# Optimization experiments

Measured on AMD Instinct MI355X. Metric: run time of the kernel, lower is better.

Reference implementation:

```python
import jax, jax.numpy as jnp
import numpy as np

EPS = 1e-06
H, D_MODEL = 16, 1024
DK = D_MODEL // H
B, S = 16, 4096


def elu_fea_map(x):
    return jax.nn.elu(x) + 1.0


def setup_inputs() -> dict:
    key = jax.random.key(0)
    ks = jax.random.split(key, 11)
    lim = 1.0 / np.sqrt(D_MODEL)
    u = lambda k, shp: jax.random.uniform(k, shp, jnp.float32, -lim, lim)
    return {
        "query": jax.random.normal(ks[0], (B, D_MODEL), jnp.float32),
        "key": jax.random.normal(ks[1], (B, S, D_MODEL), jnp.float32),
        "value": jax.random.normal(ks[2], (B, S, D_MODEL), jnp.float32),
        "Wq": u(ks[3], (D_MODEL, D_MODEL)), "bq": u(ks[4], (D_MODEL,)),
        "Wk": u(ks[5], (D_MODEL, D_MODEL)), "bk": u(ks[6], (D_MODEL,)),
        "Wv": u(ks[7], (D_MODEL, D_MODEL)), "bv": u(ks[8], (D_MODEL,)),
        "Wo": u(ks[9], (D_MODEL, D_MODEL)), "bo": u(ks[10], (D_MODEL,)),
    }


def reference(query, key, value, Wq, bq, Wk, bk, Wv, bv, Wo, bo):
    nb = query.shape[0]
    # projections; torch Linear: x @ W.T + b
    q = (query @ Wq.T + bq).reshape(nb, 1, H, DK)   # [B,1,H,D]
    k = (key @ Wk.T + bk).reshape(nb, -1, H, DK)    # [B,S,H,D]
    v = (value @ Wv.T + bv).reshape(nb, -1, H, DK)  # [B,S,H,M]
    Q = elu_fea_map(q)
    K = elu_fea_map(k)
    KV = jnp.einsum('bshd,bshm->bhdm', K, v)                      # [B,H,D,M]
    Z = 1.0 / (jnp.einsum('bshd,bhd->bsh', Q, K.sum(axis=1)) + EPS)  # [B,1,H]
    V = jnp.einsum('bshd,bhdm,bsh->bshm', Q, KV, Z)               # [B,1,H,M]
    x = V.reshape(nb, H * DK)
    return x @ Wo.T + bo
```

## Files before the change

kernel.cpp:

```cpp
#include <hip/hip_runtime.h>
#include <hip/hip_bf16.h>
#include <stdint.h>


using bf16 = __hip_bfloat16;
typedef __attribute__((ext_vector_type(8))) short short8;
typedef __attribute__((ext_vector_type(4))) float f32x4;

#define NB_B 16
#define SEQ 4096
#define DM 1024
#define NH 16
#define DKH 64

__device__ __forceinline__ void gload_lds16(const void* g, void* l) {
  __builtin_amdgcn_global_load_lds((const __attribute__((address_space(1))) void*)g,
                                   (__attribute__((address_space(3))) void*)l, 16, 0, 0);
}

__global__ __launch_bounds__(256) void conv_kernel(const float* __restrict__ src,
                                                   bf16* __restrict__ dst, long n4) {
  long i = (long)blockIdx.x * blockDim.x + threadIdx.x;
  const long stride = (long)gridDim.x * blockDim.x;
  for (; i < n4; i += stride) {
    float4 v = ((const float4*)src)[i];
    union { ushort4 u; bf16 h[4]; } o;
    o.h[0] = __float2bfloat16(v.x);
    o.h[1] = __float2bfloat16(v.y);
    o.h[2] = __float2bfloat16(v.z);
    o.h[3] = __float2bfloat16(v.w);
    ((ushort4*)dst)[i] = o.u;
  }
}

template <int KPROJ>
__global__ __launch_bounds__(256) void gemm_proj(
    const float* __restrict__ A, const bf16* __restrict__ W,
    const float* __restrict__ bias, bf16* __restrict__ outT,
    float* __restrict__ Ksum, int rowsTot, int b0, int chunk) {
  __shared__ bf16 As[128 * 64];
  __shared__ bf16 Bs[128 * 64];
  const int tid = threadIdx.x;
  const int lane = tid & 63;
  const int wid = tid >> 6;
  const int wr = wid >> 1, wc = wid & 1;
  const int wgid = (blockIdx.x & 7) * chunk + (blockIdx.x >> 3);
  const int row0 = (wgid >> 3) * 128;
  const int col0 = (wgid & 7) * 128;
  f32x4 acc[4][4] = {};

  char* AsB = (char*)As;
  const int str = tid >> 3;
  const int sslotA = ((tid & 7) ^ (str & 7));
  const int bsrc = (((lane & 7) ^ (lane >> 3)) * 8);
  const int xr = (lane & 7) << 4;
  const int lr = lane & 15;
  const int lk = (lane >> 4) * 16;

  for (int kt = 0; kt < DM / 64; ++kt) {
    const int kb = kt * 64;
#pragma unroll
    for (int i = 0; i < 4; ++i)
      gload_lds16(W + (long)(col0 + wid * 32 + i * 8 + (lane >> 3)) * DM + kb + bsrc,
                  &Bs[(wid * 4 + i) * 512]);
    float4 fa[4][2];
#pragma unroll
    for (int i = 0; i < 4; ++i) {
      const float* src = A + (long)(row0 + i * 32 + str) * DM + kb + (tid & 7) * 8;
      fa[i][0] = *(const float4*)src;
      fa[i][1] = *(const float4*)(src + 4);
    }
#pragma unroll
    for (int i = 0; i < 4; ++i) {
      union { bf16 h[8]; short8 v; } pk;
      pk.h[0] = __float2bfloat16(fa[i][0].x);
      pk.h[1] = __float2bfloat16(fa[i][0].y);
      pk.h[2] = __float2bfloat16(fa[i][0].z);
      pk.h[3] = __float2bfloat16(fa[i][0].w);
      pk.h[4] = __float2bfloat16(fa[i][1].x);
      pk.h[5] = __float2bfloat16(fa[i][1].y);
      pk.h[6] = __float2bfloat16(fa[i][1].z);
      pk.h[7] = __float2bfloat16(fa[i][1].w);
      *(short8*)(AsB + (i * 32 + str) * 128 + (sslotA << 4)) = pk.v;
    }
    __syncthreads();
#pragma unroll
    for (int kk = 0; kk < 2; ++kk) {
      short8 af[4], bfv[4];
#pragma unroll
      for (int m = 0; m < 4; ++m) {
        const int row = wr * 64 + m * 16 + lr;
        af[m] = *(const short8*)(AsB + row * 128 + ((kk * 64 + lk) ^ xr));
      }
#pragma unroll
      for (int n = 0; n < 4; ++n) {
        const int row = wc * 64 + n * 16 + lr;
        bfv[n] = *(const short8*)((char*)Bs + row * 128 + ((kk * 64 + lk) ^ xr));
      }
#pragma unroll
      for (int m = 0; m < 4; ++m)
#pragma unroll
        for (int n = 0; n < 4; ++n)
          acc[m][n] = __builtin_amdgcn_mfma_f32_16x16x32_bf16(af[m], bfv[n], acc[m][n], 0, 0, 0);
    }
    __syncthreads();
  }

  const int bglob = b0 + (row0 >> 12);
#pragma unroll
  for (int n = 0; n < 4; ++n) {
    const int colg = col0 + wc * 64 + n * 16 + (lane & 15);
    const float bv = bias[colg];
    float csum = 0.f;
#pragma unroll
    for (int m = 0; m < 4; ++m) {
      const int r = row0 + wr * 64 + m * 16 + (lane >> 4) * 4;
      union { ushort4 u; bf16 h[4]; } pk;
#pragma unroll
      for (int i = 0; i < 4; ++i) {
        float v = acc[m][n][i] + bv;
        if (KPROJ) { v = v > 0.f ? v + 1.f : __expf(v); csum += v; }
        pk.h[i] = __float2bfloat16(v);
      }
      *(ushort4*)&outT[(long)colg * rowsTot + r] = pk.u;
    }
    if (KPROJ) {
      csum += __shfl_xor(csum, 16);
      csum += __shfl_xor(csum, 32);
      if (lane < 16) atomicAdd(&Ksum[(long)bglob * DM + colg], csum);
    }
  }
}

__global__ __launch_bounds__(256) void kv_kernel(
    const bf16* __restrict__ KT, const bf16* __restrict__ VT,
    float* __restrict__ KVp, int rowsTot, int b0) {
  const int sp = blockIdx.x & 3;
  const int h = (blockIdx.x >> 2) & 15;
  const int b_loc = blockIdx.x >> 6;
  const int lane = threadIdx.x & 63;
  const int w = threadIdx.x >> 6;
  const long srow = (long)b_loc * SEQ + sp * (SEQ / 4) + ((lane >> 4) * 8);
  const bf16* Ab = KT + (long)(h * DKH + w * 16 + (lane & 15)) * rowsTot + srow;
  const bf16* Bb = VT + (long)(h * DKH + (lane & 15)) * rowsTot + srow;
  f32x4 acc[4] = {};
#pragma unroll 2
  for (int s = 0; s < SEQ / 4; s += 32) {
    short8 a = *(const short8*)(Ab + s);
#pragma unroll
    for (int n = 0; n < 4; ++n) {
      short8 bv = *(const short8*)(Bb + (long)n * 16 * rowsTot + s);
      acc[n] = __builtin_amdgcn_mfma_f32_16x16x32_bf16(a, bv, acc[n], 0, 0, 0);
    }
  }
  float* o = KVp + (((long)sp * NB_B + (b0 + b_loc)) * NH + h) * DKH * DKH;
#pragma unroll
  for (int n = 0; n < 4; ++n)
#pragma unroll
    for (int i = 0; i < 4; ++i)
      o[(w * 16 + (lane >> 4) * 4 + i) * DKH + n * 16 + (lane & 15)] = acc[n][i];
}

template <int ELU>
__global__ __launch_bounds__(256) void vecmat_kernel(
    const float* __restrict__ in, const float* __restrict__ W,
    const float* __restrict__ bias, float* __restrict__ outp) {
  const int b = blockIdx.x >> 5;
  const int n0 = (blockIdx.x & 31) * 32;
  const int lane = threadIdx.x & 63;
  const int w = threadIdx.x >> 6;
  float4 qv[4];
#pragma unroll
  for (int it = 0; it < 4; ++it)
    qv[it] = *(const float4*)&in[(long)b * DM + it * 256 + lane * 4];
#pragma unroll
  for (int j = 0; j < 8; ++j) {
    const int n = n0 + w * 8 + j;
    const float* wrow = W + (long)n * DM;
    float s = 0.f;
#pragma unroll
    for (int it = 0; it < 4; ++it) {
      float4 wv = *(const float4*)&wrow[it * 256 + lane * 4];
      s += qv[it].x * wv.x + qv[it].y * wv.y + qv[it].z * wv.z + qv[it].w * wv.w;
    }
    s += __shfl_xor(s, 1);  s += __shfl_xor(s, 2);  s += __shfl_xor(s, 4);
    s += __shfl_xor(s, 8);  s += __shfl_xor(s, 16); s += __shfl_xor(s, 32);
    if (lane == 0) {
      float v = s + bias[n];
      if (ELU) v = v > 0.f ? v + 1.f : __expf(v);
      outp[(long)b * DM + n] = v;
    }
  }
}

__global__ __launch_bounds__(256) void xcomp_kernel(
    const float* __restrict__ Q, const float* __restrict__ KVp,
    const float* __restrict__ Ksum, float* __restrict__ xb) {
  const int b = blockIdx.x;
  const int t = threadIdx.x;
  const int h = t >> 4;
  const int m0 = (t & 15) * 4;
  const float* q = Q + (long)b * DM + h * DKH;
  const float* ks = Ksum + (long)b * DM + h * DKH;
  const long kvoff = ((long)b * NH + h) * DKH * DKH;
  const long spstride = (long)NB_B * NH * DKH * DKH;
  float zden = 0.f;
#pragma unroll
  for (int d = 0; d < DKH; ++d) zden += q[d] * ks[d];
  const float z = 1.f / (zden + 1e-6f);
  float nv[4] = {0.f, 0.f, 0.f, 0.f};
  for (int d = 0; d < DKH; ++d) {
    const float qd = q[d];
#pragma unroll
    for (int j = 0; j < 4; ++j) {
      const long idx = kvoff + d * DKH + m0 + j;
      nv[j] += qd * (KVp[idx] + KVp[idx + spstride] +
                     KVp[idx + 2 * spstride] + KVp[idx + 3 * spstride]);
    }
  }
  float* xo = xb + (long)b * DM + h * DKH + m0;
#pragma unroll
  for (int j = 0; j < 4; ++j) xo[j] = nv[j] * z;
}

extern "C" void kernel_launch(void* const* d_in, const int* in_sizes, int n_in,
                              void* d_out, int out_size, void* d_ws, size_t ws_size,
                              hipStream_t stream) {
  (void)in_sizes; (void)n_in; (void)out_size;
  const float* query = (const float*)d_in[0];
  const float* key   = (const float*)d_in[1];
  const float* value = (const float*)d_in[2];
  const float* Wq = (const float*)d_in[3];
  const float* bq = (const float*)d_in[4];
  const float* Wk = (const float*)d_in[5];
  const float* bk = (const float*)d_in[6];
  const float* Wv = (const float*)d_in[7];
  const float* bv = (const float*)d_in[8];
  const float* Wo = (const float*)d_in[9];
  const float* bo = (const float*)d_in[10];
  float* out = (float*)d_out;

  char* p = (char*)d_ws;
  bf16* WkB = (bf16*)p;  p += (size_t)DM * DM * 2;
  bf16* WvB = (bf16*)p;  p += (size_t)DM * DM * 2;
  float* KVp = (float*)p; p += (size_t)4 * NB_B * NH * DKH * DKH * 4;
  float* Ksum = (float*)p; p += (size_t)NB_B * DM * 4;
  float* Q = (float*)p;  p += (size_t)NB_B * DM * 4;
  float* xb = (float*)p; p += (size_t)NB_B * DM * 4;
  const size_t fixed = (size_t)(p - (char*)d_ws);
  const size_t per_b = (size_t)2 * SEQ * DM * 2;
  if (ws_size < fixed + per_b) return;
  int nbc = (int)((ws_size - fixed) / per_b);
  if (nbc > NB_B) nbc = NB_B;
  bf16* kT = (bf16*)p; p += (size_t)nbc * SEQ * DM * 2;
  bf16* vT = (bf16*)p; p += (size_t)nbc * SEQ * DM * 2;

  hipMemsetAsync(Ksum, 0, (size_t)NB_B * DM * 4, stream);
  conv_kernel<<<512, 256, 0, stream>>>(Wk, WkB, (long)DM * DM / 4);
  conv_kernel<<<512, 256, 0, stream>>>(Wv, WvB, (long)DM * DM / 4);
  vecmat_kernel<1><<<NB_B * 32, 256, 0, stream>>>(query, Wq, bq, Q);

  for (int b0 = 0; b0 < NB_B; b0 += nbc) {
    const int nb = (NB_B - b0 < nbc) ? (NB_B - b0) : nbc;
    const int rows = nb * SEQ;
    const int nwg = (rows / 128) * 8;
    gemm_proj<1><<<nwg, 256, 0, stream>>>(key + (size_t)b0 * SEQ * DM, WkB, bk, kT, Ksum, rows, b0, nwg / 8);
    gemm_proj<0><<<nwg, 256, 0, stream>>>(value + (size_t)b0 * SEQ * DM, WvB, bv, vT, (float*)nullptr, rows, b0, nwg / 8);
    kv_kernel<<<nb * NH * 4, 256, 0, stream>>>(kT, vT, KVp, rows, b0);
  }

  xcomp_kernel<<<NB_B, 256, 0, stream>>>(Q, KVp, Ksum, xb);
  vecmat_kernel<0><<<NB_B * 32, 256, 0, stream>>>(xb, Wo, bo, out);
}
```

Before: 708.9 us.

## Double-buffer LDS tiles and prefetch A/W in projection GEMM main loop

Converts the projection GEMM's K loop to use double-buffered shared-memory tiles. The next W tile is issued via global_load_lds while MFMAs run on the current one, and A is prefetched into registers two steps ahead. One barrier per iteration with explicit vmcnt waits replaces the two __syncthreads. This aims to hide global load latency behind compute, at the cost of twice the LDS footprint, which may reduce occupancy, and fragile hand-counted waitcnt logic.

```diff
diff --git a/kernel.cpp b/kernel.cpp
--- a/kernel.cpp
+++ b/kernel.cpp
@@ -16,6 +16,15 @@
 __device__ __forceinline__ void gload_lds16(const void* g, void* l) {
   __builtin_amdgcn_global_load_lds((const __attribute__((address_space(1))) void*)g,
                                    (__attribute__((address_space(3))) void*)l, 16, 0, 0);
+}
+
+__device__ __forceinline__ short8 pack_bf16x8(float4 a, float4 b) {
+  union { bf16 h[8]; short8 v; } pk;
+  pk.h[0] = __float2bfloat16(a.x); pk.h[1] = __float2bfloat16(a.y);
+  pk.h[2] = __float2bfloat16(a.z); pk.h[3] = __float2bfloat16(a.w);
+  pk.h[4] = __float2bfloat16(b.x); pk.h[5] = __float2bfloat16(b.y);
+  pk.h[6] = __float2bfloat16(b.z); pk.h[7] = __float2bfloat16(b.w);
+  return pk.v;
 }
 
 __global__ __launch_bounds__(256) void conv_kernel(const float* __restrict__ src,
@@ -38,8 +47,8 @@
     const float* __restrict__ A, const bf16* __restrict__ W,
     const float* __restrict__ bias, bf16* __restrict__ outT,
     float* __restrict__ Ksum, int rowsTot, int b0, int chunk) {
-  __shared__ bf16 As[128 * 64];
-  __shared__ bf16 Bs[128 * 64];
+  __shared__ bf16 As[2][128 * 64];
+  __shared__ bf16 Bs[2][128 * 64];
   const int tid = threadIdx.x;
   const int lane = tid & 63;
   const int wid = tid >> 6;
@@ -49,61 +58,82 @@
   const int col0 = (wgid & 7) * 128;
   f32x4 acc[4][4] = {};
 
-  char* AsB = (char*)As;
   const int str = tid >> 3;
-  const int sslotA = ((tid & 7) ^ (str & 7));
-  const int bsrc = (((lane & 7) ^ (lane >> 3)) * 8);
+  const int sslotA = ((tid & 7) ^ (str & 7)) << 4;
+  const int acol = (tid & 7) * 8;
+  const int bsrc = ((lane & 7) ^ (lane >> 3)) * 8;
   const int xr = (lane & 7) << 4;
   const int lr = lane & 15;
   const int lk = (lane >> 4) * 16;
 
-  for (int kt = 0; kt < DM / 64; ++kt) {
-    const int kb = kt * 64;
-#pragma unroll
-    for (int i = 0; i < 4; ++i)
-      gload_lds16(W + (long)(col0 + wid * 32 + i * 8 + (lane >> 3)) * DM + kb + bsrc,
-                  &Bs[(wid * 4 + i) * 512]);
-    float4 fa[4][2];
-#pragma unroll
-    for (int i = 0; i < 4; ++i) {
-      const float* src = A + (long)(row0 + i * 32 + str) * DM + kb + (tid & 7) * 8;
-      fa[i][0] = *(const float4*)src;
-      fa[i][1] = *(const float4*)(src + 4);
-    }
-#pragma unroll
-    for (int i = 0; i < 4; ++i) {
-      union { bf16 h[8]; short8 v; } pk;
-      pk.h[0] = __float2bfloat16(fa[i][0].x);
-      pk.h[1] = __float2bfloat16(fa[i][0].y);
-      pk.h[2] = __float2bfloat16(fa[i][0].z);
-      pk.h[3] = __float2bfloat16(fa[i][0].w);
-      pk.h[4] = __float2bfloat16(fa[i][1].x);
-      pk.h[5] = __float2bfloat16(fa[i][1].y);
-      pk.h[6] = __float2bfloat16(fa[i][1].z);
-      pk.h[7] = __float2bfloat16(fa[i][1].w);
-      *(short8*)(AsB + (i * 32 + str) * 128 + (sslotA << 4)) = pk.v;
-    }
-    __syncthreads();
+  const float* Arow[4];
+#pragma unroll
+  for (int i = 0; i < 4; ++i) Arow[i] = A + (long)(row0 + i * 32 + str) * DM + acol;
+  const bf16* Wrow = W + (long)(col0 + wid * 32 + (lane >> 3)) * DM + bsrc;
+
+  float4 fa[4][2];
+#pragma unroll
+  for (int i = 0; i < 4; ++i) {
+    fa[i][0] = *(const float4*)(Arow[i]);
+    fa[i][1] = *(const float4*)(Arow[i] + 4);
+  }
+#pragma unroll
+  for (int i = 0; i < 4; ++i)
+    gload_lds16(Wrow + i * 8 * DM, &Bs[0][(wid * 4 + i) * 512]);
+#pragma unroll
+  for (int i = 0; i < 4; ++i)
+    *(short8*)((char*)As[0] + (i * 32 + str) * 128 + sslotA) = pack_bf16x8(fa[i][0], fa[i][1]);
+#pragma unroll
+  for (int i = 0; i < 4; ++i) {
+    fa[i][0] = *(const float4*)(Arow[i] + 64);
+    fa[i][1] = *(const float4*)(Arow[i] + 68);
+  }
+  asm volatile("s_waitcnt vmcnt(8) lgkmcnt(0)\n\ts_barrier" ::: "memory");
+  __builtin_amdgcn_sched_barrier(0);
+
+  for (int kt = 0; kt < 16; ++kt) {
+    const int cur = kt & 1;
+    bf16* Asc = As[cur];
+    bf16* Bsc = Bs[cur];
+    bf16* Asn = As[cur ^ 1];
+    if (kt < 15) {
+      const int kb = (kt + 1) * 64;
+#pragma unroll
+      for (int i = 0; i < 4; ++i)
+        gload_lds16(Wrow + kb + i * 8 * DM, &Bs[cur ^ 1][(wid * 4 + i) * 512]);
+    }
 #pragma unroll
     for (int kk = 0; kk < 2; ++kk) {
       short8 af[4], bfv[4];
 #pragma unroll
-      for (int m = 0; m < 4; ++m) {
-        const int row = wr * 64 + m * 16 + lr;
-        af[m] = *(const short8*)(AsB + row * 128 + ((kk * 64 + lk) ^ xr));
-      }
-#pragma unroll
-      for (int n = 0; n < 4; ++n) {
-        const int row = wc * 64 + n * 16 + lr;
-        bfv[n] = *(const short8*)((char*)Bs + row * 128 + ((kk * 64 + lk) ^ xr));
-      }
+      for (int m = 0; m < 4; ++m)
+        af[m] = *(const short8*)((char*)Asc + (wr * 64 + m * 16 + lr) * 128 + ((kk * 64 + lk) ^ xr));
+#pragma unroll
+      for (int n = 0; n < 4; ++n)
+        bfv[n] = *(const short8*)((char*)Bsc + (wc * 64 + n * 16 + lr) * 128 + ((kk * 64 + lk) ^ xr));
 #pragma unroll
       for (int m = 0; m < 4; ++m)
 #pragma unroll
         for (int n = 0; n < 4; ++n)
           acc[m][n] = __builtin_amdgcn_mfma_f32_16x16x32_bf16(af[m], bfv[n], acc[m][n], 0, 0, 0);
     }
-    __syncthreads();
+    if (kt < 15) {
+#pragma unroll
+      for (int i = 0; i < 4; ++i)
+        *(short8*)((char*)Asn + (i * 32 + str) * 128 + sslotA) = pack_bf16x8(fa[i][0], fa[i][1]);
+      if (kt < 14) {
+        const int ka = (kt + 2) * 64;
+#pragma unroll
+        for (int i = 0; i < 4; ++i) {
+          fa[i][0] = *(const float4*)(Arow[i] + ka);
+          fa[i][1] = *(const float4*)(Arow[i] + ka + 4);
+        }
+        asm volatile("s_waitcnt vmcnt(8) lgkmcnt(0)\n\ts_barrier" ::: "memory");
+      } else {
+        asm volatile("s_waitcnt vmcnt(0) lgkmcnt(0)\n\ts_barrier" ::: "memory");
+      }
+      __builtin_amdgcn_sched_barrier(0);
+    }
   }
 
   const int bglob = b0 + (row0 >> 12);
```

After: 641.5 us. 1.11x faster.

## Replace projection GEMM with 256x256 triple-buffered async-LDS pipelined kernel

Applied to the files above, without the earlier changes.

The K/V projection GEMM moves from 128x128 tiles with 256 threads to 256x256 tiles with 512 threads. Both fp32 activations and bf16 weights are staged into triple-buffered LDS through global_load_lds, and vmcnt waits let loads overlap the MFMA work. The fp32-to-bf16 conversion of A now happens after the LDS read, and MFMA phases get setprio hints and explicit barriers. This targets exposed global-load latency and raises per-block data reuse, at the cost of more LDS use, fp32 staging bandwidth in LDS, and fragile hand-counted waitcnts. The kv_kernel unroll factor also goes from 2 to 4.

```diff
diff --git a/kernel.cpp b/kernel.cpp
--- a/kernel.cpp
+++ b/kernel.cpp
@@ -16,6 +16,15 @@
 __device__ __forceinline__ void gload_lds16(const void* g, void* l) {
   __builtin_amdgcn_global_load_lds((const __attribute__((address_space(1))) void*)g,
                                    (__attribute__((address_space(3))) void*)l, 16, 0, 0);
+}
+
+__device__ __forceinline__ short8 cvt8(f32x4 a, f32x4 b) {
+  union { bf16 h[8]; short8 v; } pk;
+  pk.h[0] = __float2bfloat16(a[0]); pk.h[1] = __float2bfloat16(a[1]);
+  pk.h[2] = __float2bfloat16(a[2]); pk.h[3] = __float2bfloat16(a[3]);
+  pk.h[4] = __float2bfloat16(b[0]); pk.h[5] = __float2bfloat16(b[1]);
+  pk.h[6] = __float2bfloat16(b[2]); pk.h[7] = __float2bfloat16(b[3]);
+  return pk.v;
 }
 
 __global__ __launch_bounds__(256) void conv_kernel(const float* __restrict__ src,
@@ -34,87 +43,106 @@
 }
 
 template <int KPROJ>
-__global__ __launch_bounds__(256) void gemm_proj(
+__global__ __launch_bounds__(512, 2) void gemm256(
     const float* __restrict__ A, const bf16* __restrict__ W,
     const float* __restrict__ bias, bf16* __restrict__ outT,
     float* __restrict__ Ksum, int rowsTot, int b0, int chunk) {
-  __shared__ bf16 As[128 * 64];
-  __shared__ bf16 Bs[128 * 64];
+  __shared__ float As[3][256 * 32];
+  __shared__ bf16 Bs[3][256 * 32];
   const int tid = threadIdx.x;
   const int lane = tid & 63;
   const int wid = tid >> 6;
-  const int wr = wid >> 1, wc = wid & 1;
+  const int wr = wid >> 2;
+  const int wc = wid & 3;
   const int wgid = (blockIdx.x & 7) * chunk + (blockIdx.x >> 3);
-  const int row0 = (wgid >> 3) * 128;
-  const int col0 = (wgid & 7) * 128;
-  f32x4 acc[4][4] = {};
-
-  char* AsB = (char*)As;
-  const int str = tid >> 3;
-  const int sslotA = ((tid & 7) ^ (str & 7));
-  const int bsrc = (((lane & 7) ^ (lane >> 3)) * 8);
-  const int xr = (lane & 7) << 4;
+  const int row0 = (wgid >> 2) * 256;
+  const int col0 = (wgid & 3) * 256;
+
+  f32x4 acc[8][4] = {};
+
   const int lr = lane & 15;
-  const int lk = (lane >> 4) * 16;
-
-  for (int kt = 0; kt < DM / 64; ++kt) {
-    const int kb = kt * 64;
-#pragma unroll
-    for (int i = 0; i < 4; ++i)
-      gload_lds16(W + (long)(col0 + wid * 32 + i * 8 + (lane >> 3)) * DM + kb + bsrc,
-                  &Bs[(wid * 4 + i) * 512]);
-    float4 fa[4][2];
-#pragma unroll
-    for (int i = 0; i < 4; ++i) {
-      const float* src = A + (long)(row0 + i * 32 + str) * DM + kb + (tid & 7) * 8;
-      fa[i][0] = *(const float4*)src;
-      fa[i][1] = *(const float4*)(src + 4);
-    }
-#pragma unroll
-    for (int i = 0; i < 4; ++i) {
-      union { bf16 h[8]; short8 v; } pk;
-      pk.h[0] = __float2bfloat16(fa[i][0].x);
-      pk.h[1] = __float2bfloat16(fa[i][0].y);
-      pk.h[2] = __float2bfloat16(fa[i][0].z);
-      pk.h[3] = __float2bfloat16(fa[i][0].w);
-      pk.h[4] = __float2bfloat16(fa[i][1].x);
-      pk.h[5] = __float2bfloat16(fa[i][1].y);
-      pk.h[6] = __float2bfloat16(fa[i][1].z);
-      pk.h[7] = __float2bfloat16(fa[i][1].w);
-      *(short8*)(AsB + (i * 32 + str) * 128 + (sslotA << 4)) = pk.v;
-    }
-    __syncthreads();
-#pragma unroll
-    for (int kk = 0; kk < 2; ++kk) {
-      short8 af[4], bfv[4];
-#pragma unroll
-      for (int m = 0; m < 4; ++m) {
-        const int row = wr * 64 + m * 16 + lr;
-        af[m] = *(const short8*)(AsB + row * 128 + ((kk * 64 + lk) ^ xr));
-      }
-#pragma unroll
-      for (int n = 0; n < 4; ++n) {
-        const int row = wc * 64 + n * 16 + lr;
-        bfv[n] = *(const short8*)((char*)Bs + row * 128 + ((kk * 64 + lk) ^ xr));
-      }
-#pragma unroll
-      for (int m = 0; m < 4; ++m)
-#pragma unroll
-        for (int n = 0; n < 4; ++n)
-          acc[m][n] = __builtin_amdgcn_mfma_f32_16x16x32_bf16(af[m], bfv[n], acc[m][n], 0, 0, 0);
-    }
-    __syncthreads();
-  }
+  const int xrA = (lr & 7) << 4;
+  const int xrB = ((lr >> 1) & 3) << 4;
+  const int ksA = (lane >> 4) * 32;
+  const int ksB = (lane >> 4) * 16;
+
+  const float* Ag = A + (long)(row0 + wid * 8 + (lane >> 3)) * DM +
+                    (((lane & 7) ^ (lane >> 3)) << 2);
+  const bf16* Wg = W + (long)(col0 + wid * 16 + (lane >> 2)) * DM +
+                   (((lane & 3) ^ ((lane >> 3) & 3)) << 3);
+
+#define ISSUE_AB(ib, kt_) { \
+  _Pragma("unroll") for (int j = 0; j < 4; ++j) \
+    gload_lds16(Ag + (long)(j * 64) * DM + (kt_) * 32, \
+                (void*)((char*)As[ib] + (wid * 8 + j * 64) * 128)); \
+  _Pragma("unroll") for (int j = 0; j < 2; ++j) \
+    gload_lds16(Wg + (long)(j * 128) * DM + (kt_) * 32, \
+                (void*)((char*)Bs[ib] + (wid * 16 + j * 128) * 64)); }
+
+#define TILE_BODY(buf) { \
+  const char* AscB = (const char*)As[buf]; \
+  const char* BscB = (const char*)Bs[buf]; \
+  short8 af[4], bfv[4]; \
+  _Pragma("unroll") for (int m = 0; m < 4; ++m) { \
+    const int rb = (wr * 128 + m * 16 + lr) * 128; \
+    f32x4 a0 = *(const f32x4*)(AscB + rb + (ksA ^ xrA)); \
+    f32x4 a1 = *(const f32x4*)(AscB + rb + ((ksA + 16) ^ xrA)); \
+    af[m] = cvt8(a0, a1); } \
+  _Pragma("unroll") for (int n = 0; n < 4; ++n) \
+    bfv[n] = *(const short8*)(BscB + (wc * 64 + n * 16 + lr) * 64 + (ksB ^ xrB)); \
+  __builtin_amdgcn_sched_barrier(0); \
+  __builtin_amdgcn_s_setprio(1); \
+  _Pragma("unroll") for (int m = 0; m < 4; ++m) \
+    _Pragma("unroll") for (int n = 0; n < 4; ++n) \
+      acc[m][n] = __builtin_amdgcn_mfma_f32_16x16x32_bf16(af[m], bfv[n], acc[m][n], 0, 0, 0); \
+  __builtin_amdgcn_s_setprio(0); \
+  asm volatile("s_barrier" ::: "memory"); \
+  _Pragma("unroll") for (int m = 0; m < 4; ++m) { \
+    const int rb = (wr * 128 + (m + 4) * 16 + lr) * 128; \
+    f32x4 a0 = *(const f32x4*)(AscB + rb + (ksA ^ xrA)); \
+    f32x4 a1 = *(const f32x4*)(AscB + rb + ((ksA + 16) ^ xrA)); \
+    af[m] = cvt8(a0, a1); } \
+  asm volatile("s_barrier" ::: "memory"); \
+  __builtin_amdgcn_sched_barrier(0); \
+  __builtin_amdgcn_s_setprio(1); \
+  _Pragma("unroll") for (int m = 0; m < 4; ++m) \
+    _Pragma("unroll") for (int n = 0; n < 4; ++n) \
+      acc[m + 4][n] = __builtin_amdgcn_mfma_f32_16x16x32_bf16(af[m], bfv[n], acc[m + 4][n], 0, 0, 0); \
+  __builtin_amdgcn_s_setprio(0); \
+  asm volatile("s_barrier" ::: "memory"); }
+
+  ISSUE_AB(0, 0)
+  ISSUE_AB(1, 1)
+
+#pragma unroll 1
+  for (int kt3 = 0; kt3 < 30; kt3 += 3) {
+    ISSUE_AB(2, kt3 + 2)
+    asm volatile("s_waitcnt vmcnt(12)\n\ts_barrier" ::: "memory");
+    TILE_BODY(0)
+    ISSUE_AB(0, kt3 + 3)
+    asm volatile("s_waitcnt vmcnt(12)\n\ts_barrier" ::: "memory");
+    TILE_BODY(1)
+    ISSUE_AB(1, kt3 + 4)
+    asm volatile("s_waitcnt vmcnt(12)\n\ts_barrier" ::: "memory");
+    TILE_BODY(2)
+  }
+  asm volatile("s_waitcnt vmcnt(6)\n\ts_barrier" ::: "memory");
+  TILE_BODY(0)
+  asm volatile("s_waitcnt vmcnt(0)\n\ts_barrier" ::: "memory");
+  TILE_BODY(1)
+
+#undef ISSUE_AB
+#undef TILE_BODY
 
   const int bglob = b0 + (row0 >> 12);
 #pragma unroll
   for (int n = 0; n < 4; ++n) {
-    const int colg = col0 + wc * 64 + n * 16 + (lane & 15);
+    const int colg = col0 + wc * 64 + n * 16 + lr;
     const float bv = bias[colg];
     float csum = 0.f;
 #pragma unroll
-    for (int m = 0; m < 4; ++m) {
-      const int r = row0 + wr * 64 + m * 16 + (lane >> 4) * 4;
+    for (int m = 0; m < 8; ++m) {
+      const int r = row0 + wr * 128 + m * 16 + (lane >> 4) * 4;
       union { ushort4 u; bf16 h[4]; } pk;
 #pragma unroll
       for (int i = 0; i < 4; ++i) {
@@ -144,7 +172,7 @@
   const bf16* Ab = KT + (long)(h * DKH + w * 16 + (lane & 15)) * rowsTot + srow;
   const bf16* Bb = VT + (long)(h * DKH + (lane & 15)) * rowsTot + srow;
   f32x4 acc[4] = {};
-#pragma unroll 2
+#pragma unroll 4
   for (int s = 0; s < SEQ / 4; s += 32) {
     short8 a = *(const short8*)(Ab + s);
 #pragma unroll
@@ -263,9 +291,9 @@
   for (int b0 = 0; b0 < NB_B; b0 += nbc) {
     const int nb = (NB_B - b0 < nbc) ? (NB_B - b0) : nbc;
     const int rows = nb * SEQ;
-    const int nwg = (rows / 128) * 8;
-    gemm_proj<1><<<nwg, 256, 0, stream>>>(key + (size_t)b0 * SEQ * DM, WkB, bk, kT, Ksum, rows, b0, nwg / 8);
-    gemm_proj<0><<<nwg, 256, 0, stream>>>(value + (size_t)b0 * SEQ * DM, WvB, bv, vT, (float*)nullptr, rows, b0, nwg / 8);
+    const int nwg = (rows / 256) * 4;
+    gemm256<1><<<nwg, 512, 0, stream>>>(key + (size_t)b0 * SEQ * DM, WkB, bk, kT, Ksum, rows, b0, nwg / 8);
+    gemm256<0><<<nwg, 512, 0, stream>>>(value + (size_t)b0 * SEQ * DM, WvB, bv, vT, (float*)nullptr, rows, b0, nwg / 8);
     kv_kernel<<<nb * NH * 4, 256, 0, stream>>>(kT, vT, KVp, rows, b0);
   }
 
```

New measurement: 693.8 us. -2.1%, faster.

## Software-pipeline projection GEMM with double-buffered W tiles and prefetched A

Applied to the files above, without the earlier changes.

Restructures the K/V projection GEMM main loop. The fp32 A tile for step t+2 is prefetched into registers while W tiles are double-buffered in LDS through async global-to-LDS loads, with explicit vmcnt waits and barriers replacing the two syncthreads per iteration. It also raises MFMA issue priority with setprio, sets launch bounds for 3 blocks per CU, and bumps the kv_kernel unroll to 4. The goal is to hide global memory latency behind MFMA work, at the cost of extra register and LDS pressure. The hand-written waitcnt counts are fragile if the compiler reorders memory operations.

```diff
diff --git a/kernel.cpp b/kernel.cpp
--- a/kernel.cpp
+++ b/kernel.cpp
@@ -16,6 +16,15 @@
 __device__ __forceinline__ void gload_lds16(const void* g, void* l) {
   __builtin_amdgcn_global_load_lds((const __attribute__((address_space(1))) void*)g,
                                    (__attribute__((address_space(3))) void*)l, 16, 0, 0);
+}
+
+__device__ __forceinline__ short8 cvt8(float4 a, float4 b) {
+  union { bf16 h[8]; short8 v; } pk;
+  pk.h[0] = __float2bfloat16(a.x); pk.h[1] = __float2bfloat16(a.y);
+  pk.h[2] = __float2bfloat16(a.z); pk.h[3] = __float2bfloat16(a.w);
+  pk.h[4] = __float2bfloat16(b.x); pk.h[5] = __float2bfloat16(b.y);
+  pk.h[6] = __float2bfloat16(b.z); pk.h[7] = __float2bfloat16(b.w);
+  return pk.v;
 }
 
 __global__ __launch_bounds__(256) void conv_kernel(const float* __restrict__ src,
@@ -34,82 +43,102 @@
 }
 
 template <int KPROJ>
-__global__ __launch_bounds__(256) void gemm_proj(
+__global__ __launch_bounds__(256, 3) void gemm128(
     const float* __restrict__ A, const bf16* __restrict__ W,
     const float* __restrict__ bias, bf16* __restrict__ outT,
     float* __restrict__ Ksum, int rowsTot, int b0, int chunk) {
   __shared__ bf16 As[128 * 64];
-  __shared__ bf16 Bs[128 * 64];
+  __shared__ bf16 Bs[2][128 * 64];
   const int tid = threadIdx.x;
   const int lane = tid & 63;
   const int wid = tid >> 6;
-  const int wr = wid >> 1, wc = wid & 1;
+  const int wr = wid >> 1;
+  const int wc = wid & 1;
   const int wgid = (blockIdx.x & 7) * chunk + (blockIdx.x >> 3);
   const int row0 = (wgid >> 3) * 128;
   const int col0 = (wgid & 7) * 128;
+
   f32x4 acc[4][4] = {};
 
-  char* AsB = (char*)As;
-  const int str = tid >> 3;
-  const int sslotA = ((tid & 7) ^ (str & 7));
-  const int bsrc = (((lane & 7) ^ (lane >> 3)) * 8);
+  const int lr = lane & 15;
   const int xr = (lane & 7) << 4;
-  const int lr = lane & 15;
   const int lk = (lane >> 4) * 16;
 
-  for (int kt = 0; kt < DM / 64; ++kt) {
-    const int kb = kt * 64;
-#pragma unroll
-    for (int i = 0; i < 4; ++i)
-      gload_lds16(W + (long)(col0 + wid * 32 + i * 8 + (lane >> 3)) * DM + kb + bsrc,
-                  &Bs[(wid * 4 + i) * 512]);
-    float4 fa[4][2];
-#pragma unroll
-    for (int i = 0; i < 4; ++i) {
-      const float* src = A + (long)(row0 + i * 32 + str) * DM + kb + (tid & 7) * 8;
-      fa[i][0] = *(const float4*)src;
-      fa[i][1] = *(const float4*)(src + 4);
-    }
-#pragma unroll
-    for (int i = 0; i < 4; ++i) {
-      union { bf16 h[8]; short8 v; } pk;
-      pk.h[0] = __float2bfloat16(fa[i][0].x);
-      pk.h[1] = __float2bfloat16(fa[i][0].y);
-      pk.h[2] = __float2bfloat16(fa[i][0].z);
-      pk.h[3] = __float2bfloat16(fa[i][0].w);
-      pk.h[4] = __float2bfloat16(fa[i][1].x);
-      pk.h[5] = __float2bfloat16(fa[i][1].y);
-      pk.h[6] = __float2bfloat16(fa[i][1].z);
-      pk.h[7] = __float2bfloat16(fa[i][1].w);
-      *(short8*)(AsB + (i * 32 + str) * 128 + (sslotA << 4)) = pk.v;
-    }
-    __syncthreads();
+  const int ra = tid >> 1;
+  const float* Ag = A + (long)(row0 + ra) * DM + (tid & 1) * 32;
+  const int awbase = ra * 128;
+  const int akey = (ra & 7) << 4;
+  const int ac0 = (tid & 1) * 4;
+
+  const bf16* Wg = W + (long)(col0 + wid * 32 + (lane >> 3)) * DM +
+                   ((lane & 7) ^ (lane >> 3)) * 8;
+  const int sdstB = wid * 32 * 64;
+
+  float4 fa[8];
+
+#define A_ISSUE(T_) { \
+  _Pragma("unroll") for (int j = 0; j < 4; ++j) { \
+    fa[2 * j]     = *(const float4*)(Ag + (T_) * 64 + j * 8); \
+    fa[2 * j + 1] = *(const float4*)(Ag + (T_) * 64 + j * 8 + 4); } }
+
+#define A_WRITE() { \
+  _Pragma("unroll") for (int j = 0; j < 4; ++j) \
+    *(short8*)((char*)As + awbase + (((ac0 + j) * 16) ^ akey)) = \
+        cvt8(fa[2 * j], fa[2 * j + 1]); }
+
+#define B_STAGE(buf, T_) { \
+  _Pragma("unroll") for (int j = 0; j < 4; ++j) \
+    gload_lds16(Wg + (long)j * 8 * DM + (T_) * 64, (void*)&Bs[buf][sdstB + j * 512]); }
+
+  A_ISSUE(0)
+  B_STAGE(0, 0)
+  A_WRITE()
+  A_ISSUE(1)
+  B_STAGE(1, 1)
+  asm volatile("s_waitcnt vmcnt(12) lgkmcnt(0)\n\ts_barrier" ::: "memory");
+
+#pragma unroll 1
+  for (int t = 0; t < 16; ++t) {
+    const char* Bc = (const char*)Bs[t & 1];
 #pragma unroll
     for (int kk = 0; kk < 2; ++kk) {
       short8 af[4], bfv[4];
 #pragma unroll
-      for (int m = 0; m < 4; ++m) {
-        const int row = wr * 64 + m * 16 + lr;
-        af[m] = *(const short8*)(AsB + row * 128 + ((kk * 64 + lk) ^ xr));
-      }
-#pragma unroll
-      for (int n = 0; n < 4; ++n) {
-        const int row = wc * 64 + n * 16 + lr;
-        bfv[n] = *(const short8*)((char*)Bs + row * 128 + ((kk * 64 + lk) ^ xr));
-      }
+      for (int m = 0; m < 4; ++m)
+        af[m] = *(const short8*)((char*)As + (wr * 64 + m * 16 + lr) * 128 +
+                                 ((kk * 64 + lk) ^ xr));
+#pragma unroll
+      for (int n = 0; n < 4; ++n)
+        bfv[n] = *(const short8*)(Bc + (wc * 64 + n * 16 + lr) * 128 +
+                                  ((kk * 64 + lk) ^ xr));
+      __builtin_amdgcn_s_setprio(1);
 #pragma unroll
       for (int m = 0; m < 4; ++m)
 #pragma unroll
         for (int n = 0; n < 4; ++n)
           acc[m][n] = __builtin_amdgcn_mfma_f32_16x16x32_bf16(af[m], bfv[n], acc[m][n], 0, 0, 0);
-    }
-    __syncthreads();
-  }
+      __builtin_amdgcn_s_setprio(0);
+    }
+    if (t < 15) {
+      asm volatile("s_waitcnt lgkmcnt(0)\n\ts_barrier" ::: "memory");
+      A_WRITE()
+      if (t < 14) {
+        A_ISSUE(t + 2)
+        B_STAGE(t & 1, t + 2)
+        asm volatile("s_waitcnt vmcnt(12) lgkmcnt(0)\n\ts_barrier" ::: "memory");
+      } else {
+        asm volatile("s_waitcnt vmcnt(0) lgkmcnt(0)\n\ts_barrier" ::: "memory");
+      }
+    }
+  }
+#undef A_ISSUE
+#undef A_WRITE
+#undef B_STAGE
 
   const int bglob = b0 + (row0 >> 12);
 #pragma unroll
   for (int n = 0; n < 4; ++n) {
-    const int colg = col0 + wc * 64 + n * 16 + (lane & 15);
+    const int colg = col0 + wc * 64 + n * 16 + lr;
     const float bv = bias[colg];
     float csum = 0.f;
 #pragma unroll
@@ -144,7 +173,7 @@
   const bf16* Ab = KT + (long)(h * DKH + w * 16 + (lane & 15)) * rowsTot + srow;
   const bf16* Bb = VT + (long)(h * DKH + (lane & 15)) * rowsTot + srow;
   f32x4 acc[4] = {};
-#pragma unroll 2
+#pragma unroll 4
   for (int s = 0; s < SEQ / 4; s += 32) {
     short8 a = *(const short8*)(Ab + s);
 #pragma unroll
@@ -264,8 +293,8 @@
     const int nb = (NB_B - b0 < nbc) ? (NB_B - b0) : nbc;
     const int rows = nb * SEQ;
     const int nwg = (rows / 128) * 8;
-    gemm_proj<1><<<nwg, 256, 0, stream>>>(key + (size_t)b0 * SEQ * DM, WkB, bk, kT, Ksum, rows, b0, nwg / 8);
-    gemm_proj<0><<<nwg, 256, 0, stream>>>(value + (size_t)b0 * SEQ * DM, WvB, bv, vT, (float*)nullptr, rows, b0, nwg / 8);
+    gemm128<1><<<nwg, 256, 0, stream>>>(key + (size_t)b0 * SEQ * DM, WkB, bk, kT, Ksum, rows, b0, nwg / 8);
+    gemm128<0><<<nwg, 256, 0, stream>>>(value + (size_t)b0 * SEQ * DM, WvB, bv, vT, (float*)nullptr, rows, b0, nwg / 8);
     kv_kernel<<<nb * NH * 4, 256, 0, stream>>>(kT, vT, KVp, rows, b0);
   }
 
```

Measured after the change: 843.4 us. 19.0% more time.
